# Kernel optimization log

Measured on AMD Instinct MI355X. Metric: run time of the kernel, lower is better.

Reference implementation:

```python
import jax, jax.numpy as jnp
import numpy as np

D_IN = 384
HID = 384
D_OUT = 384

def _kaiming(key, fan_in, fan_out):
    return jax.random.normal(key, (fan_in, fan_out), dtype=jnp.float32) * np.sqrt(2.0 / fan_in)

def setup_inputs() -> dict:
    key = jax.random.key(0)
    ks = jax.random.split(key, 12)
    B, O, T = 8, 1024, 8192
    obj_vecs = jax.random.normal(ks[0], (B, O, D_IN), dtype=jnp.float32)
    pred_vecs = jax.random.normal(ks[1], (B, T, D_IN), dtype=jnp.float32)
    edges = jax.random.randint(ks[2], (B, T, 2), 0, O, dtype=jnp.int64)
    # gconv1: [3D -> H -> 2H + Dout]; gconv2: [H -> H -> Dout]
    w1a = _kaiming(ks[3], 3 * D_IN, HID); b1a = jnp.zeros((HID,), jnp.float32)
    w1b = _kaiming(ks[4], HID, 2 * HID + D_OUT); b1b = jnp.zeros((2 * HID + D_OUT,), jnp.float32)
    w2a = _kaiming(ks[5], HID, HID); b2a = jnp.zeros((HID,), jnp.float32)
    w2b = _kaiming(ks[6], HID, D_OUT); b2b = jnp.zeros((D_OUT,), jnp.float32)
    return {"obj_vecs": obj_vecs, "pred_vecs": pred_vecs, "edges": edges,
            "w1a": w1a, "b1a": b1a, "w1b": w1b, "b1b": b1b,
            "w2a": w2a, "b2a": b2a, "w2b": w2b, "b2b": b2b}

def _gconv_forward(obj_vecs, pred_vecs, edges, w1a, b1a, w1b, b1b, w2a, b2a, w2b, b2b):
    B, O, D = obj_vecs.shape
    s_idx = edges[:, :, 0]  # (B, T)
    o_idx = edges[:, :, 1]
    batch = jnp.arange(B)[:, None]
    subj = obj_vecs[batch, s_idx]  # (B, T, D) gather
    objt = obj_vecs[batch, o_idx]
    triple = jnp.concatenate([subj, pred_vecs, objt], axis=-1)  # (B, T, 3D)
    h = jax.nn.relu(triple @ w1a + b1a)
    t = jax.nn.relu(h @ w1b + b1b)  # (B, T, 2H + Dout)
    new_s = t[:, :, :HID]
    new_p = t[:, :, HID:HID + D_OUT]
    new_o = t[:, :, HID + D_OUT:]
    # scatter_add per batch into (O, H) buffers
    def agg(si, oi, vs, vo):
        return jnp.zeros((O, HID), vs.dtype).at[si].add(vs).at[oi].add(vo)
    pooled = jax.vmap(agg)(s_idx, o_idx, new_s, new_o)  # (B, O, H)
    pooled = pooled / jnp.linalg.norm(pooled)  # global Frobenius norm, as in torch .norm()
    out_obj = jax.nn.relu(jax.nn.relu(pooled @ w2a + b2a) @ w2b + b2b)
    return out_obj, new_p

def reference(obj_vecs, pred_vecs, edges, w1a, b1a, w1b, b1b, w2a, b2a, w2b, b2b):
    return _gconv_forward(obj_vecs, pred_vecs, edges, w1a, b1a, w1b, b1b, w2a, b2a, w2b, b2b)
```

## Files before the change

kernel.cpp:

```cpp
#include <hip/hip_runtime.h>
#include <hip/hip_bf16.h>

#define NB 8
#define NT 8192
#define NO 1024
#define DD 384
#define K1 1152
#define M1 65536
#define MO 8192

typedef __attribute__((ext_vector_type(8))) short bf16x8;
typedef __attribute__((ext_vector_type(4))) float f32x4;
typedef __attribute__((ext_vector_type(4))) unsigned short u16x4;

__device__ __forceinline__ unsigned short f2bf(float f) {
    union { float f; unsigned u; } v; v.f = f;
    unsigned r = v.u + 0x7FFFu + ((v.u >> 16) & 1u);
    return (unsigned short)(r >> 16);
}
__device__ __forceinline__ float bf2f(unsigned short h) {
    union { unsigned u; float f; } v; v.u = ((unsigned)h) << 16;
    return v.f;
}
__device__ __forceinline__ bf16x8 pack8(f32x4 a, f32x4 b) {
    bf16x8 r;
    r[0] = (short)f2bf(a[0]); r[1] = (short)f2bf(a[1]);
    r[2] = (short)f2bf(a[2]); r[3] = (short)f2bf(a[3]);
    r[4] = (short)f2bf(b[0]); r[5] = (short)f2bf(b[1]);
    r[6] = (short)f2bf(b[2]); r[7] = (short)f2bf(b[3]);
    return r;
}
__device__ __forceinline__ void gload16(const void* g, void* l) {
    __builtin_amdgcn_global_load_lds(
        (const __attribute__((address_space(1))) unsigned int*)g,
        (__attribute__((address_space(3))) unsigned int*)l, 16, 0, 0);
}

__global__ void k_cvt4(const float* __restrict__ s, unsigned short* __restrict__ d, int n) {
    int i = (blockIdx.x * blockDim.x + threadIdx.x) * 4;
    if (i >= n) return;
    f32x4 v = *(const f32x4*)(s + i);
    u16x4 o;
    o[0] = f2bf(v[0]); o[1] = f2bf(v[1]); o[2] = f2bf(v[2]); o[3] = f2bf(v[3]);
    *(u16x4*)(d + i) = o;
}
__global__ void k_tr(const float* __restrict__ s, unsigned short* __restrict__ d, int K, int N) {
    int k = blockIdx.x;
    int n = blockIdx.y * blockDim.x + threadIdx.x;
    if (n < N) d[n * K + k] = f2bf(s[k * N + n]);
}

__global__ void k_ss1(const float* __restrict__ p, float* __restrict__ partial, int n4) {
    __shared__ float wsum[4];
    int stride = gridDim.x * blockDim.x;
    float s = 0.f;
    for (int i = blockIdx.x * blockDim.x + threadIdx.x; i < n4; i += stride) {
        f32x4 v = *(const f32x4*)(p + i * 4);
        s += v[0] * v[0] + v[1] * v[1] + v[2] * v[2] + v[3] * v[3];
    }
#pragma unroll
    for (int off = 32; off; off >>= 1) s += __shfl_down(s, off, 64);
    if ((threadIdx.x & 63) == 0) wsum[threadIdx.x >> 6] = s;
    __syncthreads();
    if (threadIdx.x == 0)
        partial[blockIdx.x] = wsum[0] + wsum[1] + wsum[2] + wsum[3];
}
__global__ void k_ss2(const float* __restrict__ partial, float* __restrict__ o) {
    float s = partial[threadIdx.x];
#pragma unroll
    for (int off = 32; off; off >>= 1) s += __shfl_down(s, off, 64);
    __shared__ float w0, w1;
    if (threadIdx.x == 0) w0 = s;
    if (threadIdx.x == 64) w1 = s;
    __syncthreads();
    if (threadIdx.x == 0) o[0] = w0 + w1;
}
__global__ void k_normcvt(const float* __restrict__ p, const float* __restrict__ ss,
                          unsigned short* __restrict__ o) {
    int i = (blockIdx.x * blockDim.x + threadIdx.x) * 8;
    float s = rsqrtf(ss[0]);
    f32x4 a = *(const f32x4*)(p + i), b = *(const f32x4*)(p + i + 4);
    a *= s; b *= s;
    *(bf16x8*)(o + i) = pack8(a, b);
}

__global__ void k_hist(const int* __restrict__ edges, int* __restrict__ cnt) {
    int i = blockIdx.x * 256 + threadIdx.x;
    int2 e = *(const int2*)&edges[(size_t)i * 2];
    int b = i >> 13;
    atomicAdd(&cnt[(b << 10) + e.x], 1);
    atomicAdd(&cnt[(b << 10) + e.y], 1);
}
__global__ void k_scan(const int* __restrict__ cnt, int* __restrict__ offs) {
    __shared__ int a[1024];
    int b = blockIdx.x, t = threadIdx.x;
    int own = cnt[(b << 10) + t];
    a[t] = own;
    __syncthreads();
    for (int s = 1; s < 1024; s <<= 1) {
        int v = (t >= s) ? a[t - s] : 0;
        __syncthreads();
        a[t] += v;
        __syncthreads();
    }
    offs[(b << 10) + t] = a[t] - own;
}
__global__ void k_fill(const int* __restrict__ edges, const int* __restrict__ offs,
                       int* __restrict__ cur, int* __restrict__ elist) {
    int i = blockIdx.x * 256 + threadIdx.x;
    int2 e = *(const int2*)&edges[(size_t)i * 2];
    int b = i >> 13, t = i & (NT - 1);
    int ps = atomicAdd(&cur[(b << 10) + e.x], 1);
    elist[(b << 14) + offs[(b << 10) + e.x] + ps] = t * 2;
    int po = atomicAdd(&cur[(b << 10) + e.y], 1);
    elist[(b << 14) + offs[(b << 10) + e.y] + po] = t * 2 + 1;
}
__global__ void k_pool(const unsigned short* __restrict__ sob, const int* __restrict__ cnt,
                       const int* __restrict__ offs, const int* __restrict__ elist,
                       float* __restrict__ pooled) {
    int w = (blockIdx.x * 256 + threadIdx.x) >> 6;
    int lane = threadIdx.x & 63;
    if (lane >= 48) return;
    int b = w >> 10, o = w & (NO - 1);
    int len = cnt[(b << 10) + o];
    const int* lst = elist + (b << 14) + offs[(b << 10) + o];
    f32x4 a0 = {0.f, 0.f, 0.f, 0.f}, a1 = {0.f, 0.f, 0.f, 0.f};
    for (int j = 0; j < len; ++j) {
        int e = lst[j];
        int t = e >> 1, tag = e & 1;
        bf16x8 v = *(const bf16x8*)(sob + ((size_t)((b << 13) + t)) * 768 + tag * DD + lane * 8);
        a0[0] += bf2f((unsigned short)v[0]); a0[1] += bf2f((unsigned short)v[1]);
        a0[2] += bf2f((unsigned short)v[2]); a0[3] += bf2f((unsigned short)v[3]);
        a1[0] += bf2f((unsigned short)v[4]); a1[1] += bf2f((unsigned short)v[5]);
        a1[2] += bf2f((unsigned short)v[6]); a1[3] += bf2f((unsigned short)v[7]);
    }
    float* dst = pooled + ((size_t)((b << 10) + o)) * DD + lane * 8;
    *(f32x4*)dst = a0;
    *(f32x4*)(dst + 4) = a1;
}

template <int STAGE, int EPI>
__launch_bounds__(512, 2)
__global__ void gemm_k(const unsigned short* __restrict__ Abf,
                       const unsigned short* __restrict__ objb,
                       const float* __restrict__ predf,
                       const int* __restrict__ edges,
                       const unsigned short* __restrict__ Bt,
                       const float* __restrict__ bias,
                       unsigned short* __restrict__ outb,
                       float* __restrict__ outf,
                       int K, int ldC,
                       int bt_row0, int bt_step, int out_col0, int col_step)
{
    const int tid = threadIdx.x;
    const int lane = tid & 63;
    const int m0 = blockIdx.x * 128;
    const int bt0 = bt_row0 + (int)blockIdx.y * bt_step;
    const int col0 = out_col0 + (int)blockIdx.y * col_step;

    __shared__ unsigned short At[128 * 64];
    __shared__ unsigned short Bl[384 * 64];
    __shared__ int eidx[128][2];

    if (STAGE == 1) {
        if (tid < 128) {
            int2 e = *(const int2*)&edges[(size_t)(m0 + tid) * 2];
            eidx[tid][0] = e.x;
            eidx[tid][1] = e.y;
        }
        __syncthreads();
    }

    const int rb = tid >> 3;
    const int c8 = ((tid & 7) ^ (rb & 7)) * 8;

    int er0[2], er1[2];
    if (STAGE == 1) {
        const int bb = (m0 >> 13) << 10;
#pragma unroll
        for (int i = 0; i < 2; ++i) {
            er0[i] = bb + eidx[i * 64 + rb][0];
            er1[i] = bb + eidx[i * 64 + rb][1];
        }
    }

    f32x4 acc[4][6];
#pragma unroll
    for (int i = 0; i < 4; ++i)
#pragma unroll
        for (int j = 0; j < 6; ++j) acc[i][j] = (f32x4){0.f, 0.f, 0.f, 0.f};

    const int wid = tid >> 6, wm = wid >> 2, wn = wid & 3;
    const int l16 = lane & 15, lg = lane >> 4;

    for (int kk = 0; kk < K; kk += 64) {
#pragma unroll
        for (int i = 0; i < 6; ++i)
            gload16(Bt + (size_t)(bt0 + i * 64 + rb) * K + kk + c8, Bl + i * 4096 + tid * 8);
        if (STAGE == 0) {
#pragma unroll
            for (int i = 0; i < 2; ++i)
                gload16(Abf + (size_t)(m0 + i * 64 + rb) * K + kk + c8, At + i * 4096 + tid * 8);
        } else {
            const int seg = kk / DD;
            const int ko = kk - seg * DD;
            if (seg == 1) {
#pragma unroll
                for (int i = 0; i < 2; ++i) {
                    const float* p = predf + (size_t)(m0 + i * 64 + rb) * DD + ko + c8;
                    *(bf16x8*)(At + i * 4096 + tid * 8) = pack8(*(const f32x4*)p, *(const f32x4*)(p + 4));
                }
            } else if (seg == 0) {
#pragma unroll
                for (int i = 0; i < 2; ++i)
                    gload16(objb + (size_t)er0[i] * DD + ko + c8, At + i * 4096 + tid * 8);
            } else {
#pragma unroll
                for (int i = 0; i < 2; ++i)
                    gload16(objb + (size_t)er1[i] * DD + ko + c8, At + i * 4096 + tid * 8);
            }
        }
        __syncthreads();
#pragma unroll
        for (int kt = 0; kt < 2; ++kt) {
            const int cs = ((kt * 4 + lg) ^ (l16 & 7)) * 8;
            bf16x8 af[4], bfr[6];
#pragma unroll
            for (int mt = 0; mt < 4; ++mt)
                af[mt] = *(const bf16x8*)(At + (wm * 64 + mt * 16 + l16) * 64 + cs);
#pragma unroll
            for (int nt = 0; nt < 6; ++nt)
                bfr[nt] = *(const bf16x8*)(Bl + (wn * 96 + nt * 16 + l16) * 64 + cs);
#pragma unroll
            for (int mt = 0; mt < 4; ++mt)
#pragma unroll
                for (int nt = 0; nt < 6; ++nt)
                    acc[mt][nt] = __builtin_amdgcn_mfma_f32_16x16x32_bf16(af[mt], bfr[nt], acc[mt][nt], 0, 0, 0);
        }
        __syncthreads();
    }

#pragma unroll
    for (int nt = 0; nt < 6; ++nt) {
        int gn = wn * 96 + nt * 16 + l16;
        float bv = bias[bt0 + gn];
#pragma unroll
        for (int mt = 0; mt < 4; ++mt) {
            int rbase = wm * 64 + mt * 16 + lg * 4;
#pragma unroll
            for (int rg = 0; rg < 4; ++rg) {
                int gr = m0 + rbase + rg;
                float v = fmaxf(acc[mt][nt][rg] + bv, 0.0f);
                if (EPI == 0) outb[(size_t)gr * ldC + col0 + gn] = f2bf(v);
                else          outf[(size_t)gr * ldC + col0 + gn] = v;
            }
        }
    }
}

extern "C" void kernel_launch(void* const* d_in, const int* in_sizes, int n_in,
                              void* d_out, int out_size, void* d_ws, size_t ws_size,
                              hipStream_t stream)
{
    const float* obj  = (const float*)d_in[0];
    const float* pred = (const float*)d_in[1];
    const int* edges  = (const int*)d_in[2];
    const float* w1a  = (const float*)d_in[3];
    const float* b1a  = (const float*)d_in[4];
    const float* w1b  = (const float*)d_in[5];
    const float* b1b  = (const float*)d_in[6];
    const float* w2a  = (const float*)d_in[7];
    const float* b2a  = (const float*)d_in[8];
    const float* w2b  = (const float*)d_in[9];
    const float* b2b  = (const float*)d_in[10];

    float* out_obj = (float*)d_out;
    float* newp    = out_obj + (size_t)MO * DD;
    unsigned short* sob = (unsigned short*)newp;

    unsigned short* objb = (unsigned short*)d_ws;
    unsigned short* w1aT = objb + (size_t)NB * NO * DD;
    unsigned short* w1bT = w1aT + (size_t)DD * K1;
    unsigned short* w2aT = w1bT + (size_t)K1 * DD;
    unsigned short* w2bT = w2aT + (size_t)DD * DD;
    unsigned short* hbuf = w2bT + (size_t)DD * DD;
    float* pooled = (float*)(hbuf + (size_t)M1 * DD);
    float* sumsq  = pooled + (size_t)MO * DD;
    unsigned short* hid2 = (unsigned short*)(sumsq + 4);
    int* cnt   = (int*)(hid2 + (size_t)MO * DD);
    int* cur   = cnt + NB * NO;
    int* offs  = cur + NB * NO;
    int* elist = offs + NB * NO;
    float* partial = (float*)(elist + 2 * M1);
    unsigned short* poolb = objb;

    hipLaunchKernelGGL(k_cvt4, dim3(3072), dim3(256), 0, stream, obj, objb, NB * NO * DD);
    hipLaunchKernelGGL(k_tr, dim3(K1, 3), dim3(128), 0, stream, w1a, w1aT, K1, DD);
    hipLaunchKernelGGL(k_tr, dim3(DD, 9), dim3(128), 0, stream, w1b, w1bT, DD, K1);
    hipLaunchKernelGGL(k_tr, dim3(DD, 3), dim3(128), 0, stream, w2a, w2aT, DD, DD);
    hipLaunchKernelGGL(k_tr, dim3(DD, 3), dim3(128), 0, stream, w2b, w2bT, DD, DD);
    hipMemsetAsync(cnt, 0, 2 * NB * NO * sizeof(int), stream);

    hipLaunchKernelGGL((gemm_k<1, 0>), dim3(M1 / 128, 1), dim3(512), 0, stream,
                       (const unsigned short*)nullptr, objb, pred, edges,
                       w1aT, b1a, hbuf, (float*)nullptr, K1, DD, 0, 0, 0, 0);

    hipLaunchKernelGGL((gemm_k<0, 0>), dim3(M1 / 128, 2), dim3(512), 0, stream,
                       hbuf, (const unsigned short*)nullptr, (const float*)nullptr, (const int*)nullptr,
                       w1bT, b1b, sob, (float*)nullptr, DD, 2 * DD, 0, 2 * DD, 0, DD);

    hipLaunchKernelGGL(k_hist, dim3(256), dim3(256), 0, stream, edges, cnt);
    hipLaunchKernelGGL(k_scan, dim3(8), dim3(1024), 0, stream, cnt, offs);
    hipLaunchKernelGGL(k_fill, dim3(256), dim3(256), 0, stream, edges, offs, cur, elist);
    hipLaunchKernelGGL(k_pool, dim3(2048), dim3(256), 0, stream, sob, cnt, offs, elist, pooled);

    hipLaunchKernelGGL((gemm_k<0, 2>), dim3(M1 / 128, 1), dim3(512), 0, stream,
                       hbuf, (const unsigned short*)nullptr, (const float*)nullptr, (const int*)nullptr,
                       w1bT, b1b, (unsigned short*)nullptr, newp, DD, DD, DD, 0, 0, 0);

    hipLaunchKernelGGL(k_ss1, dim3(128), dim3(256), 0, stream, pooled, partial, MO * DD / 4);
    hipLaunchKernelGGL(k_ss2, dim3(1), dim3(128), 0, stream, partial, sumsq);
    hipLaunchKernelGGL(k_normcvt, dim3(1536), dim3(256), 0, stream, pooled, sumsq, poolb);

    hipLaunchKernelGGL((gemm_k<0, 0>), dim3(MO / 128, 1), dim3(512), 0, stream,
                       poolb, (const unsigned short*)nullptr, (const float*)nullptr, (const int*)nullptr,
                       w2aT, b2a, hid2, (float*)nullptr, DD, DD, 0, 0, 0, 0);

    hipLaunchKernelGGL((gemm_k<0, 2>), dim3(MO / 128, 1), dim3(512), 0, stream,
                       hid2, (const unsigned short*)nullptr, (const float*)nullptr, (const int*)nullptr,
                       w2bT, b2b, (unsigned short*)nullptr, out_obj, DD, DD, 0, 0, 0, 0);
}
```

Baseline: 305.5 us.

## Prefetch next A tile into registers during MFMA and unroll pooling gather by two

The GEMM loop now issues the next K-slice's A-operand loads (gathered object rows or fp32 predicate rows) into registers before the MFMA work on the current tile. After compute it writes them to LDS and loads the next B tile. The aim is to hide global gather latency behind matrix math. The pooling kernel processes two edge entries per iteration with separate accumulators so more loads are in flight. Costs are extra registers, which may pressure occupancy at 512 threads with launch_bounds 2, and B loads that remain unoverlapped after compute.

Result: slower. 311.8 us (+2.1%).

```diff
diff --git a/kernel.cpp b/kernel.cpp
--- a/kernel.cpp
+++ b/kernel.cpp
@@ -125,15 +125,30 @@
     int len = cnt[(b << 10) + o];
     const int* lst = elist + (b << 14) + offs[(b << 10) + o];
     f32x4 a0 = {0.f, 0.f, 0.f, 0.f}, a1 = {0.f, 0.f, 0.f, 0.f};
-    for (int j = 0; j < len; ++j) {
-        int e = lst[j];
-        int t = e >> 1, tag = e & 1;
-        bf16x8 v = *(const bf16x8*)(sob + ((size_t)((b << 13) + t)) * 768 + tag * DD + lane * 8);
-        a0[0] += bf2f((unsigned short)v[0]); a0[1] += bf2f((unsigned short)v[1]);
-        a0[2] += bf2f((unsigned short)v[2]); a0[3] += bf2f((unsigned short)v[3]);
-        a1[0] += bf2f((unsigned short)v[4]); a1[1] += bf2f((unsigned short)v[5]);
-        a1[2] += bf2f((unsigned short)v[6]); a1[3] += bf2f((unsigned short)v[7]);
-    }
+    f32x4 c0 = {0.f, 0.f, 0.f, 0.f}, c1 = {0.f, 0.f, 0.f, 0.f};
+    int j = 0;
+    for (; j + 1 < len; j += 2) {
+        int e0 = lst[j], e1 = lst[j + 1];
+        bf16x8 v0 = *(const bf16x8*)(sob + ((size_t)((b << 13) + (e0 >> 1))) * 768 + (e0 & 1) * DD + lane * 8);
+        bf16x8 v1 = *(const bf16x8*)(sob + ((size_t)((b << 13) + (e1 >> 1))) * 768 + (e1 & 1) * DD + lane * 8);
+        a0[0] += bf2f((unsigned short)v0[0]); a0[1] += bf2f((unsigned short)v0[1]);
+        a0[2] += bf2f((unsigned short)v0[2]); a0[3] += bf2f((unsigned short)v0[3]);
+        a1[0] += bf2f((unsigned short)v0[4]); a1[1] += bf2f((unsigned short)v0[5]);
+        a1[2] += bf2f((unsigned short)v0[6]); a1[3] += bf2f((unsigned short)v0[7]);
+        c0[0] += bf2f((unsigned short)v1[0]); c0[1] += bf2f((unsigned short)v1[1]);
+        c0[2] += bf2f((unsigned short)v1[2]); c0[3] += bf2f((unsigned short)v1[3]);
+        c1[0] += bf2f((unsigned short)v1[4]); c1[1] += bf2f((unsigned short)v1[5]);
+        c1[2] += bf2f((unsigned short)v1[6]); c1[3] += bf2f((unsigned short)v1[7]);
+    }
+    if (j < len) {
+        int e0 = lst[j];
+        bf16x8 v0 = *(const bf16x8*)(sob + ((size_t)((b << 13) + (e0 >> 1))) * 768 + (e0 & 1) * DD + lane * 8);
+        a0[0] += bf2f((unsigned short)v0[0]); a0[1] += bf2f((unsigned short)v0[1]);
+        a0[2] += bf2f((unsigned short)v0[2]); a0[3] += bf2f((unsigned short)v0[3]);
+        a1[0] += bf2f((unsigned short)v0[4]); a1[1] += bf2f((unsigned short)v0[5]);
+        a1[2] += bf2f((unsigned short)v0[6]); a1[3] += bf2f((unsigned short)v0[7]);
+    }
+    a0 += c0; a1 += c1;
     float* dst = pooled + ((size_t)((b << 10) + o)) * DD + lane * 8;
     *(f32x4*)dst = a0;
     *(f32x4*)(dst + 4) = a1;
@@ -193,34 +208,52 @@
     const int wid = tid >> 6, wm = wid >> 2, wn = wid & 3;
     const int l16 = lane & 15, lg = lane >> 4;
 
+#pragma unroll
+    for (int i = 0; i < 6; ++i)
+        gload16(Bt + (size_t)(bt0 + i * 64 + rb) * K + c8, Bl + i * 4096 + tid * 8);
+    if (STAGE == 0) {
+#pragma unroll
+        for (int i = 0; i < 2; ++i)
+            gload16(Abf + (size_t)(m0 + i * 64 + rb) * K + c8, At + i * 4096 + tid * 8);
+    } else {
+#pragma unroll
+        for (int i = 0; i < 2; ++i)
+            gload16(objb + (size_t)er0[i] * DD + c8, At + i * 4096 + tid * 8);
+    }
+    __syncthreads();
+
     for (int kk = 0; kk < K; kk += 64) {
-#pragma unroll
-        for (int i = 0; i < 6; ++i)
-            gload16(Bt + (size_t)(bt0 + i * 64 + rb) * K + kk + c8, Bl + i * 4096 + tid * 8);
-        if (STAGE == 0) {
-#pragma unroll
-            for (int i = 0; i < 2; ++i)
-                gload16(Abf + (size_t)(m0 + i * 64 + rb) * K + kk + c8, At + i * 4096 + tid * 8);
-        } else {
-            const int seg = kk / DD;
-            const int ko = kk - seg * DD;
-            if (seg == 1) {
-#pragma unroll
-                for (int i = 0; i < 2; ++i) {
-                    const float* p = predf + (size_t)(m0 + i * 64 + rb) * DD + ko + c8;
-                    *(bf16x8*)(At + i * 4096 + tid * 8) = pack8(*(const f32x4*)p, *(const f32x4*)(p + 4));
+        const int kn = kk + 64;
+        const bool has_next = (kn < K);
+        bf16x8 pa[2];
+        f32x4 pf[2][2];
+        int nseg = 0;
+        if (has_next) {
+            if (STAGE == 0) {
+#pragma unroll
+                for (int i = 0; i < 2; ++i)
+                    pa[i] = *(const bf16x8*)(Abf + (size_t)(m0 + i * 64 + rb) * K + kn + c8);
+            } else {
+                nseg = kn / DD;
+                const int ko = kn - nseg * DD;
+                if (nseg == 1) {
+#pragma unroll
+                    for (int i = 0; i < 2; ++i) {
+                        const float* p = predf + (size_t)(m0 + i * 64 + rb) * DD + ko + c8;
+                        pf[i][0] = *(const f32x4*)p;
+                        pf[i][1] = *(const f32x4*)(p + 4);
+                    }
+                } else if (nseg == 0) {
+#pragma unroll
+                    for (int i = 0; i < 2; ++i)
+                        pa[i] = *(const bf16x8*)(objb + (size_t)er0[i] * DD + ko + c8);
+                } else {
+#pragma unroll
+                    for (int i = 0; i < 2; ++i)
+                        pa[i] = *(const bf16x8*)(objb + (size_t)er1[i] * DD + ko + c8);
                 }
-            } else if (seg == 0) {
-#pragma unroll
-                for (int i = 0; i < 2; ++i)
-                    gload16(objb + (size_t)er0[i] * DD + ko + c8, At + i * 4096 + tid * 8);
-            } else {
-#pragma unroll
-                for (int i = 0; i < 2; ++i)
-                    gload16(objb + (size_t)er1[i] * DD + ko + c8, At + i * 4096 + tid * 8);
             }
         }
-        __syncthreads();
 #pragma unroll
         for (int kt = 0; kt < 2; ++kt) {
             const int cs = ((kt * 4 + lg) ^ (l16 & 7)) * 8;
@@ -238,6 +271,21 @@
                     acc[mt][nt] = __builtin_amdgcn_mfma_f32_16x16x32_bf16(af[mt], bfr[nt], acc[mt][nt], 0, 0, 0);
         }
         __syncthreads();
+        if (has_next) {
+            if (STAGE == 1 && nseg == 1) {
+#pragma unroll
+                for (int i = 0; i < 2; ++i)
+                    *(bf16x8*)(At + i * 4096 + tid * 8) = pack8(pf[i][0], pf[i][1]);
+            } else {
+#pragma unroll
+                for (int i = 0; i < 2; ++i)
+                    *(bf16x8*)(At + i * 4096 + tid * 8) = pa[i];
+            }
+#pragma unroll
+            for (int i = 0; i < 6; ++i)
+                gload16(Bt + (size_t)(bt0 + i * 64 + rb) * K + kn + c8, Bl + i * 4096 + tid * 8);
+            __syncthreads();
+        }
     }
 
 #pragma unroll
```
